# Kernel optimization log

Measured on AMD Instinct MI355X. Metric: run time of the kernel, lower is better.

The kernel has to match this reference:

```python
import jax, jax.numpy as jnp
import numpy as np

N = 50000
E = 800000
IN_C = 256
HID = 256
HEADS = 8
HEAD_C = HID // HEADS
OUT_C = 64
NEG_SLOPE = 0.2  # PyG GATConv default leaky_relu slope


def _glorot(key, shape):
    fan_in = shape[0]
    return jax.random.normal(key, shape, dtype=jnp.float32) / jnp.sqrt(jnp.float32(fan_in))


def setup_inputs() -> dict:
    key = jax.random.key(0)
    ks = jax.random.split(key, 10)
    x = jax.random.normal(ks[0], (N, IN_C), dtype=jnp.float32)
    edge_index = jax.random.randint(ks[1], (2, E), 0, N, dtype=jnp.int32)
    return {
        "x": x,
        "edge_index": edge_index,
        "w1": _glorot(ks[2], (IN_C, HID)),
        "b1": jnp.zeros((HID,), jnp.float32),
        "w_att": _glorot(ks[3], (HID, HEADS * HEAD_C)),
        "att_src": jax.random.normal(ks[4], (HEADS, HEAD_C), dtype=jnp.float32) * 0.1,
        "att_dst": jax.random.normal(ks[5], (HEADS, HEAD_C), dtype=jnp.float32) * 0.1,
        "b_att": jnp.zeros((HEADS * HEAD_C,), jnp.float32),
        "w_mu": _glorot(ks[6], (HID, OUT_C)),
        "b_mu": jnp.zeros((OUT_C,), jnp.float32),
        "w_ls": _glorot(ks[7], (HID, OUT_C)),
        "b_ls": jnp.zeros((OUT_C,), jnp.float32),
    }


def _with_self_loops(edge_index, n):
    loop = jnp.arange(n, dtype=edge_index.dtype)
    src = jnp.concatenate([edge_index[0], loop])
    dst = jnp.concatenate([edge_index[1], loop])
    return src, dst


def gcn_conv(x, w, b, src, dst, n):
    # PyG GCNConv: x' = D^{-1/2} (A+I) D^{-1/2} X W + b
    h = x @ w  # [N, F]
    deg = jax.ops.segment_sum(jnp.ones_like(dst, dtype=h.dtype), dst, num_segments=n)
    dinv = jax.lax.rsqrt(jnp.maximum(deg, 1.0))  # deg >= 1 due to self loops
    norm = dinv[src] * dinv[dst]  # [E']
    msg = h[src] * norm[:, None]
    return jax.ops.segment_sum(msg, dst, num_segments=n) + b


def gat_conv(x, w, att_src, att_dst, b, src, dst, n):
    # PyG GATConv (concat heads, self loops, leaky_relu 0.2, edge softmax by dst)
    h = (x @ w).reshape(n, HEADS, HEAD_C)  # [N, H, C]
    a_src = jnp.einsum('nhc,hc->nh', h, att_src)  # [N, H]
    a_dst = jnp.einsum('nhc,hc->nh', h, att_dst)
    e = jax.nn.leaky_relu(a_src[src] + a_dst[dst], NEG_SLOPE)  # [E', H]
    m = jax.ops.segment_max(e, dst, num_segments=n)  # [N, H]
    e = jnp.exp(e - m[dst])
    s = jax.ops.segment_sum(e, dst, num_segments=n)  # [N, H]
    alpha = e / s[dst]  # [E', H]
    out = jax.ops.segment_sum(h[src] * alpha[:, :, None], dst, num_segments=n)
    return out.reshape(n, HEADS * HEAD_C) + b


def reference(x, edge_index, w1, b1, w_att, att_src, att_dst, b_att, w_mu, b_mu, w_ls, b_ls):
    n = x.shape[0]
    src, dst = _with_self_loops(edge_index, n)
    h = jax.nn.gelu(gcn_conv(x, w1, b1, src, dst, n))
    # dropout is identity at inference
    h = jax.nn.relu(gat_conv(h, w_att, att_src, att_dst, b_att, src, dst, n))
    mu = gcn_conv(h, w_mu, b_mu, src, dst, n)
    logstd = gcn_conv(h, w_ls, b_ls, src, dst, n)
    return mu, logstd
```

## Files before the change

### kernel.cpp

```cpp
#include <hip/hip_runtime.h>

#define NN 50000
#define EE 800000
#define ET (EE + NN)
#define HID 256
#define NH 8
#define HC 32
#define OC 64
#define PC 128

typedef unsigned int u32;
typedef unsigned short u16s;
typedef __bf16 bf16;
typedef _Float16 f16;
typedef __attribute__((ext_vector_type(8))) __bf16 bf16x8;
typedef __attribute__((ext_vector_type(8))) _Float16 f16x8;
typedef __attribute__((ext_vector_type(4))) _Float16 f16x4;
typedef __attribute__((ext_vector_type(4))) float f32x4;

static __device__ __forceinline__ float geluf(float x){
  float t = tanhf(0.7978845608028654f*(x + 0.044715f*x*x*x));
  return 0.5f*x*(1.0f+t);
}
static __device__ __forceinline__ float leakyf(float x){
  return x > 0.0f ? x : 0.2f*x;
}

__global__ void k_init(u32* cnt, u32* counter){
  int i = blockIdx.x*blockDim.x + threadIdx.x;
  if (i < NN) cnt[i] = 1u;
  if (i == 0) counter[0] = 0u;
}
__global__ void k_count(const int* __restrict__ dst, u32* __restrict__ cnt){
  int e = blockIdx.x*blockDim.x + threadIdx.x;
  if (e < EE) atomicAdd(&cnt[dst[e]], 1u);
}
__global__ void k_alloc(const u32* __restrict__ cnt, u32* counter,
                        u32* __restrict__ start, u32* __restrict__ pos,
                        float* __restrict__ dinv){
  int n = blockIdx.x*blockDim.x + threadIdx.x;
  const int lane = threadIdx.x & 63;
  u32 c = (n < NN) ? cnt[n] : 0u;
  u32 pre = c;
  #pragma unroll
  for (int off=1; off<64; off<<=1){
    u32 v = __shfl_up(pre, off);
    if (lane >= off) pre += v;
  }
  u32 tot = __shfl(pre, 63);
  u32 base = 0;
  if (lane == 63) base = atomicAdd(counter, tot);
  base = __shfl(base, 63);
  if (n < NN){
    u32 s = base + pre - c;
    start[n] = s; pos[n] = s;
    dinv[n] = rsqrtf((float)c);
  }
}
__global__ void k_fill(const int* __restrict__ src, const int* __restrict__ dst,
                       u32* __restrict__ pos, u16s* __restrict__ col,
                       const float* __restrict__ dinv, float* __restrict__ nrmE){
  int e = blockIdx.x*blockDim.x + threadIdx.x;
  if (e < ET){
    int s, d;
    if (e < EE){ s = src[e]; d = dst[e]; } else { s = d = e - EE; }
    u32 idx = atomicAdd(&pos[d], 1u);
    col[idx] = (u16s)s;
    nrmE[idx] = dinv[s] * dinv[d];
  }
}

template<int NC>
__global__ void k_wsplit_bf(const float* __restrict__ W, bf16* __restrict__ Whi, bf16* __restrict__ Wlo){
  int e = blockIdx.x*blockDim.x + threadIdx.x;
  if (e >= NC*HID) return;
  int c = e / HID, k = e % HID;
  float w = W[(size_t)k*NC + c];
  bf16 hi = (bf16)w;
  bf16 lo = (bf16)(w - (float)hi);
  Whi[(size_t)c*HID + k] = hi;
  Wlo[(size_t)c*HID + k] = lo;
}
template<int NC>
__global__ void k_wsplit_f16(const float* __restrict__ W, f16* __restrict__ Whi, f16* __restrict__ Wlo, int coff){
  int e = blockIdx.x*blockDim.x + threadIdx.x;
  if (e >= NC*HID) return;
  int c = e / HID, k = e % HID;
  float w = W[(size_t)k*NC + c];
  f16 hi = (f16)w;
  f16 lo = (f16)(w - (float)hi);
  Whi[(size_t)(c+coff)*HID + k] = hi;
  Wlo[(size_t)(c+coff)*HID + k] = lo;
}

template<int NC, int NF, int MR>
__global__ __launch_bounds__(256) void k_gemm_f32A(const float* __restrict__ A,
    const bf16* __restrict__ Whi, const bf16* __restrict__ Wlo, f16* __restrict__ Cout){
  const int tid = threadIdx.x;
  const int w = tid >> 6, lane = tid & 63;
  const int r = lane & 15, g = lane >> 4;
  const int row0 = blockIdx.x * (MR*16);
  const int wcol = w * (NF*16);
  f32x4 acc[MR][NF];
  #pragma unroll
  for (int m=0;m<MR;++m)
    #pragma unroll
    for (int j=0;j<NF;++j){ f32x4 z = {0.f,0.f,0.f,0.f}; acc[m][j] = z; }
  #pragma unroll
  for (int kk=0; kk<8; ++kk){
    const int k0 = kk*32 + g*8;
    bf16x8 ahi[MR], alo[MR];
    #pragma unroll
    for (int m=0;m<MR;++m){
      const int row = row0 + m*16 + r;
      float af[8] = {0.f,0.f,0.f,0.f,0.f,0.f,0.f,0.f};
      if (row < NN){
        const float* ap = A + (size_t)row*HID + k0;
        const float4 u0 = *(const float4*)ap;
        const float4 u1 = *(const float4*)(ap+4);
        af[0]=u0.x; af[1]=u0.y; af[2]=u0.z; af[3]=u0.w;
        af[4]=u1.x; af[5]=u1.y; af[6]=u1.z; af[7]=u1.w;
      }
      #pragma unroll
      for (int i=0;i<8;++i){
        bf16 h = (bf16)af[i];
        ahi[m][i] = h;
        alo[m][i] = (bf16)(af[i] - (float)h);
      }
    }
    #pragma unroll
    for (int j=0;j<NF;++j){
      const int c = wcol + j*16 + r;
      const size_t off = (size_t)c*HID + k0;
      const bf16x8 wh = *(const bf16x8*)(Whi + off);
      const bf16x8 wl = *(const bf16x8*)(Wlo + off);
      #pragma unroll
      for (int m=0;m<MR;++m){
        acc[m][j] = __builtin_amdgcn_mfma_f32_16x16x32_bf16(ahi[m], wh, acc[m][j], 0, 0, 0);
        acc[m][j] = __builtin_amdgcn_mfma_f32_16x16x32_bf16(ahi[m], wl, acc[m][j], 0, 0, 0);
        acc[m][j] = __builtin_amdgcn_mfma_f32_16x16x32_bf16(alo[m], wh, acc[m][j], 0, 0, 0);
      }
    }
  }
  #pragma unroll
  for (int j=0;j<NF;++j){
    const int c = wcol + j*16 + r;
    #pragma unroll
    for (int m=0;m<MR;++m){
      #pragma unroll
      for (int q=0;q<4;++q){
        const int row = row0 + m*16 + g*4 + q;
        if (row < NN) Cout[(size_t)row*NC + c] = (f16)acc[m][j][q];
      }
    }
  }
}

template<int NC, int NF, int MR>
__global__ __launch_bounds__(256) void k_gemm_f16A(const f16* __restrict__ A,
    const f16* __restrict__ Whi, const f16* __restrict__ Wlo, f16* __restrict__ Cout){
  const int tid = threadIdx.x;
  const int w = tid >> 6, lane = tid & 63;
  const int r = lane & 15, g = lane >> 4;
  const int row0 = blockIdx.x * (MR*16);
  const int wcol = w * (NF*16);
  f32x4 acc[MR][NF];
  #pragma unroll
  for (int m=0;m<MR;++m)
    #pragma unroll
    for (int j=0;j<NF;++j){ f32x4 z = {0.f,0.f,0.f,0.f}; acc[m][j] = z; }
  #pragma unroll
  for (int kk=0; kk<8; ++kk){
    const int k0 = kk*32 + g*8;
    f16x8 a[MR];
    #pragma unroll
    for (int m=0;m<MR;++m){
      const int row = row0 + m*16 + r;
      f16x8 z = {0,0,0,0,0,0,0,0};
      a[m] = (row < NN) ? *(const f16x8*)(A + (size_t)row*HID + k0) : z;
    }
    #pragma unroll
    for (int j=0;j<NF;++j){
      const int c = wcol + j*16 + r;
      const size_t off = (size_t)c*HID + k0;
      const f16x8 wh = *(const f16x8*)(Whi + off);
      const f16x8 wl = *(const f16x8*)(Wlo + off);
      #pragma unroll
      for (int m=0;m<MR;++m){
        acc[m][j] = __builtin_amdgcn_mfma_f32_16x16x32_f16(a[m], wh, acc[m][j], 0, 0, 0);
        acc[m][j] = __builtin_amdgcn_mfma_f32_16x16x32_f16(a[m], wl, acc[m][j], 0, 0, 0);
      }
    }
  }
  #pragma unroll
  for (int j=0;j<NF;++j){
    const int c = wcol + j*16 + r;
    #pragma unroll
    for (int m=0;m<MR;++m){
      #pragma unroll
      for (int q=0;q<4;++q){
        const int row = row0 + m*16 + g*4 + q;
        if (row < NN) Cout[(size_t)row*NC + c] = (f16)acc[m][j][q];
      }
    }
  }
}

__global__ __launch_bounds__(256) void k_gemm_att(const f16* __restrict__ A,
    const f16* __restrict__ Whi, const f16* __restrict__ Wlo,
    const float* __restrict__ atts, const float* __restrict__ attd,
    f16* __restrict__ Cout, float* __restrict__ a_src, float* __restrict__ a_dst){
  const int tid = threadIdx.x;
  const int w = tid >> 6, lane = tid & 63;
  const int r = lane & 15, g = lane >> 4;
  const int row0 = blockIdx.x * 64;
  const int wcol = w * 64;
  f32x4 acc[4][4];
  #pragma unroll
  for (int m=0;m<4;++m)
    #pragma unroll
    for (int j=0;j<4;++j){ f32x4 z = {0.f,0.f,0.f,0.f}; acc[m][j] = z; }
  #pragma unroll
  for (int kk=0; kk<8; ++kk){
    const int k0 = kk*32 + g*8;
    f16x8 a[4];
    #pragma unroll
    for (int m=0;m<4;++m){
      const int row = row0 + m*16 + r;
      f16x8 z = {0,0,0,0,0,0,0,0};
      a[m] = (row < NN) ? *(const f16x8*)(A + (size_t)row*HID + k0) : z;
    }
    #pragma unroll
    for (int j=0;j<4;++j){
      const int c = wcol + j*16 + r;
      const size_t off = (size_t)c*HID + k0;
      const f16x8 wh = *(const f16x8*)(Whi + off);
      const f16x8 wl = *(const f16x8*)(Wlo + off);
      #pragma unroll
      for (int m=0;m<4;++m){
        acc[m][j] = __builtin_amdgcn_mfma_f32_16x16x32_f16(a[m], wh, acc[m][j], 0, 0, 0);
        acc[m][j] = __builtin_amdgcn_mfma_f32_16x16x32_f16(a[m], wl, acc[m][j], 0, 0, 0);
      }
    }
  }
  float atv[4], adv[4];
  #pragma unroll
  for (int j=0;j<4;++j){ atv[j] = atts[wcol+j*16+r]; adv[j] = attd[wcol+j*16+r]; }
  #pragma unroll
  for (int m=0;m<4;++m){
    float ps[2][4] = {{0,0,0,0},{0,0,0,0}};
    float pd[2][4] = {{0,0,0,0},{0,0,0,0}};
    #pragma unroll
    for (int j=0;j<4;++j){
      const int c = wcol + j*16 + r;
      const int hl = j >> 1;
      #pragma unroll
      for (int q=0;q<4;++q){
        const int row = row0 + m*16 + g*4 + q;
        const float v = acc[m][j][q];
        if (row < NN) Cout[(size_t)row*HID + c] = (f16)v;
        ps[hl][q] = fmaf(v, atv[j], ps[hl][q]);
        pd[hl][q] = fmaf(v, adv[j], pd[hl][q]);
      }
    }
    #pragma unroll
    for (int hl=0;hl<2;++hl)
      #pragma unroll
      for (int q=0;q<4;++q){
        float s = ps[hl][q], d = pd[hl][q];
        s += __shfl_xor(s,1); s += __shfl_xor(s,2); s += __shfl_xor(s,4); s += __shfl_xor(s,8);
        d += __shfl_xor(d,1); d += __shfl_xor(d,2); d += __shfl_xor(d,4); d += __shfl_xor(d,8);
        if (r == 0){
          const int row = row0 + m*16 + g*4 + q;
          if (row < NN){
            a_src[(size_t)row*NH + 2*w + hl] = s;
            a_dst[(size_t)row*NH + 2*w + hl] = d;
          }
        }
      }
  }
}

__global__ __launch_bounds__(256) void k_aggH(const f16* __restrict__ feat,
    const u16s* __restrict__ col, const u32* __restrict__ start, const u32* __restrict__ cnt,
    const float* __restrict__ nrmE, const float* __restrict__ bias, f16* __restrict__ out){
  const int n = (int)((blockIdx.x*blockDim.x + threadIdx.x) >> 6);
  if (n >= NN) return;
  const int lane = threadIdx.x & 63;
  const u32 b = start[n], e = b + cnt[n];
  const int fo = lane*4;
  float a0=0.f,a1=0.f,a2=0.f,a3=0.f;
  u32 s0 = col[b];
  float w0 = nrmE[b];
  f16x4 v0 = *(const f16x4*)(feat + (size_t)s0*HID + fo);
  for (u32 k=b+1; k<e; ++k){
    const u32 s1 = col[k];
    const float w1 = nrmE[k];
    const f16x4 v1 = *(const f16x4*)(feat + (size_t)s1*HID + fo);
    a0 = fmaf(w0, (float)v0.x, a0);
    a1 = fmaf(w0, (float)v0.y, a1);
    a2 = fmaf(w0, (float)v0.z, a2);
    a3 = fmaf(w0, (float)v0.w, a3);
    v0 = v1; w0 = w1;
  }
  a0 = fmaf(w0, (float)v0.x, a0);
  a1 = fmaf(w0, (float)v0.y, a1);
  a2 = fmaf(w0, (float)v0.z, a2);
  a3 = fmaf(w0, (float)v0.w, a3);
  const float4 bv = *(const float4*)(bias + fo);
  f16x4 o;
  o.x = (f16)geluf(a0 + bv.x);
  o.y = (f16)geluf(a1 + bv.y);
  o.z = (f16)geluf(a2 + bv.z);
  o.w = (f16)geluf(a3 + bv.w);
  *(f16x4*)(out + (size_t)n*HID + fo) = o;
}

__global__ __launch_bounds__(256) void k_gat_fused(const f16* __restrict__ gfeat,
    const u16s* __restrict__ col, const u32* __restrict__ start, const u32* __restrict__ cnt,
    const float* __restrict__ a_src, const float* __restrict__ a_dst,
    const float* __restrict__ b_att, f16* __restrict__ h2){
  const int n = (int)((blockIdx.x*blockDim.x + threadIdx.x) >> 6);
  if (n >= NN) return;
  const int lane = threadIdx.x & 63;
  const int head = lane >> 3;
  const int fo = lane*4;
  const u32 b = start[n], e = b + cnt[n];
  const float ad = a_dst[(size_t)n*NH + head];
  float a0=0.f,a1=0.f,a2=0.f,a3=0.f,sp=0.f;
  u32 s0 = col[b];
  float as0 = a_src[(size_t)s0*NH + head];
  f16x4 v0 = *(const f16x4*)(gfeat + (size_t)s0*HID + fo);
  for (u32 k=b+1; k<e; ++k){
    const u32 s1 = col[k];
    const float as1 = a_src[(size_t)s1*NH + head];
    const f16x4 v1 = *(const f16x4*)(gfeat + (size_t)s1*HID + fo);
    const float p = expf(leakyf(as0 + ad));
    sp += p;
    a0 = fmaf(p, (float)v0.x, a0);
    a1 = fmaf(p, (float)v0.y, a1);
    a2 = fmaf(p, (float)v0.z, a2);
    a3 = fmaf(p, (float)v0.w, a3);
    v0 = v1; as0 = as1;
  }
  const float p = expf(leakyf(as0 + ad));
  sp += p;
  a0 = fmaf(p, (float)v0.x, a0);
  a1 = fmaf(p, (float)v0.y, a1);
  a2 = fmaf(p, (float)v0.z, a2);
  a3 = fmaf(p, (float)v0.w, a3);
  const float inv_s = 1.f / sp;
  const float4 bv = *(const float4*)(b_att + fo);
  f16x4 o;
  o.x = (f16)fmaxf(fmaf(a0, inv_s, bv.x), 0.f);
  o.y = (f16)fmaxf(fmaf(a1, inv_s, bv.y), 0.f);
  o.z = (f16)fmaxf(fmaf(a2, inv_s, bv.z), 0.f);
  o.w = (f16)fmaxf(fmaf(a3, inv_s, bv.w), 0.f);
  *(f16x4*)(h2 + (size_t)n*HID + fo) = o;
}

__global__ __launch_bounds__(256) void k_agg_out(const f16* __restrict__ p,
    const u16s* __restrict__ col, const u32* __restrict__ start, const u32* __restrict__ cnt,
    const float* __restrict__ nrmE, const float* __restrict__ b_mu, const float* __restrict__ b_ls,
    float* __restrict__ out){
  const int n = (int)((blockIdx.x*blockDim.x + threadIdx.x) >> 6);
  if (n >= NN) return;
  const int lane = threadIdx.x & 63;
  const int q4 = lane >> 4, l4 = lane & 15;
  const int fo = l4*8;
  const u32 b = start[n], c = cnt[n];
  float acc[8] = {0.f,0.f,0.f,0.f,0.f,0.f,0.f,0.f};
  u32 i0 = (u32)q4;
  bool v0 = i0 < c;
  u32 idx0 = b + (v0 ? i0 : 0u);
  u32 s0 = col[idx0];
  float nrm0 = v0 ? nrmE[idx0] : 0.f;
  f16x8 f0 = *(const f16x8*)(p + (size_t)s0*PC + fo);
  for (u32 k=4; k<c; k+=4){
    const u32 i1 = k + (u32)q4;
    const bool v1 = i1 < c;
    const u32 idx1 = b + (v1 ? i1 : 0u);
    const u32 s1 = col[idx1];
    const float nrm1 = v1 ? nrmE[idx1] : 0.f;
    const f16x8 f1 = *(const f16x8*)(p + (size_t)s1*PC + fo);
    #pragma unroll
    for (int j=0;j<8;++j) acc[j] = fmaf(nrm0, (float)f0[j], acc[j]);
    f0 = f1; nrm0 = nrm1;
  }
  #pragma unroll
  for (int j=0;j<8;++j) acc[j] = fmaf(nrm0, (float)f0[j], acc[j]);
  #pragma unroll
  for (int j=0;j<8;++j){
    acc[j] += __shfl_xor(acc[j], 16);
    acc[j] += __shfl_xor(acc[j], 32);
  }
  if (q4 == 0){
    if (l4 < 8){
      const int cc = fo;
      float4 o0 = make_float4(acc[0]+b_mu[cc], acc[1]+b_mu[cc+1], acc[2]+b_mu[cc+2], acc[3]+b_mu[cc+3]);
      float4 o1 = make_float4(acc[4]+b_mu[cc+4], acc[5]+b_mu[cc+5], acc[6]+b_mu[cc+6], acc[7]+b_mu[cc+7]);
      *(float4*)(out + (size_t)n*OC + cc) = o0;
      *(float4*)(out + (size_t)n*OC + cc + 4) = o1;
    } else {
      const int cc = fo - OC;
      float* o = out + (size_t)NN*OC + (size_t)n*OC + cc;
      float4 o0 = make_float4(acc[0]+b_ls[cc], acc[1]+b_ls[cc+1], acc[2]+b_ls[cc+2], acc[3]+b_ls[cc+3]);
      float4 o1 = make_float4(acc[4]+b_ls[cc+4], acc[5]+b_ls[cc+5], acc[6]+b_ls[cc+6], acc[7]+b_ls[cc+7]);
      *(float4*)o = o0;
      *(float4*)(o + 4) = o1;
    }
  }
}

extern "C" void kernel_launch(void* const* d_in, const int* in_sizes, int n_in,
                              void* d_out, int out_size, void* d_ws, size_t ws_size,
                              hipStream_t stream){
  const float* x    = (const float*)d_in[0];
  const int*   ei   = (const int*)d_in[1];
  const float* w1   = (const float*)d_in[2];
  const float* b1   = (const float*)d_in[3];
  const float* watt = (const float*)d_in[4];
  const float* atts = (const float*)d_in[5];
  const float* attd = (const float*)d_in[6];
  const float* batt = (const float*)d_in[7];
  const float* wmu  = (const float*)d_in[8];
  const float* bmu  = (const float*)d_in[9];
  const float* wls  = (const float*)d_in[10];
  const float* bls  = (const float*)d_in[11];
  const int* esrc = ei;
  const int* edst = ei + EE;

  char* p = (char*)d_ws;
  f16* bufA = (f16*)p;  p += (size_t)NN*HID*2;
  f16* bufB = (f16*)p;  p += (size_t)NN*HID*2;
  f16* bufC = (f16*)p;  p += (size_t)NN*HID*2;
  float* nrmE = (float*)p; p += (size_t)ET*4;
  bf16* w1hi = (bf16*)p; p += (size_t)HID*HID*2;
  bf16* w1lo = (bf16*)p; p += (size_t)HID*HID*2;
  f16* wahi  = (f16*)p;  p += (size_t)HID*HID*2;
  f16* walo  = (f16*)p;  p += (size_t)HID*HID*2;
  f16* wchi  = (f16*)p;  p += (size_t)PC*HID*2;
  f16* wclo  = (f16*)p;  p += (size_t)PC*HID*2;
  float* dinv = (float*)p; p += (size_t)NN*4;
  float* asr  = (float*)p; p += (size_t)NN*NH*4;
  float* ads  = (float*)p; p += (size_t)NN*NH*4;
  u32*   cnt  = (u32*)p;   p += (size_t)NN*4;
  u32*   start= (u32*)p;   p += (size_t)NN*4;
  u32*   pos  = (u32*)p;   p += (size_t)NN*4;
  u32*   counter = (u32*)p; p += 256;
  u16s*  colU = (u16s*)p;  p += (size_t)ET*2;

  const int TB = 256;
  k_init <<<(NN+TB-1)/TB, TB, 0, stream>>>(cnt, counter);
  k_count<<<(EE+TB-1)/TB, TB, 0, stream>>>(edst, cnt);
  k_alloc<<<(NN+TB-1)/TB, TB, 0, stream>>>(cnt, counter, start, pos, dinv);
  k_fill <<<(ET+TB-1)/TB, TB, 0, stream>>>(esrc, edst, pos, colU, dinv, nrmE);
  k_wsplit_bf<HID><<<(HID*HID+TB-1)/TB, TB, 0, stream>>>(w1, w1hi, w1lo);
  k_wsplit_f16<HID><<<(HID*HID+TB-1)/TB, TB, 0, stream>>>(watt, wahi, walo, 0);
  k_wsplit_f16<OC> <<<(OC*HID+TB-1)/TB, TB, 0, stream>>>(wmu, wchi, wclo, 0);
  k_wsplit_f16<OC> <<<(OC*HID+TB-1)/TB, TB, 0, stream>>>(wls, wchi, wclo, OC);

  const int NWB = NN/4;
  const int G64 = (NN + 63)/64;
  k_gemm_f32A<HID,4,4><<<G64, TB, 0, stream>>>(x, w1hi, w1lo, bufA);
  k_aggH<<<NWB, TB, 0, stream>>>(bufA, colU, start, cnt, nrmE, b1, bufB);
  k_gemm_att<<<G64, TB, 0, stream>>>(bufB, wahi, walo, atts, attd, bufC, asr, ads);
  k_gat_fused<<<NWB, TB, 0, stream>>>(bufC, colU, start, cnt, asr, ads, batt, bufA);
  k_gemm_f16A<PC,2,4><<<G64, TB, 0, stream>>>(bufA, wchi, wclo, bufB);
  k_agg_out<<<NWB, TB, 0, stream>>>(bufB, colU, start, cnt, nrmE, bmu, bls, (float*)d_out);
}
```

Before: 451.5 us.

## Convert x to fp16, merge weight splits, and unroll gather loops by two

```diff
diff --git a/kernel.cpp b/kernel.cpp
--- a/kernel.cpp
+++ b/kernel.cpp
@@ -11,9 +11,7 @@
 
 typedef unsigned int u32;
 typedef unsigned short u16s;
-typedef __bf16 bf16;
 typedef _Float16 f16;
-typedef __attribute__((ext_vector_type(8))) __bf16 bf16x8;
 typedef __attribute__((ext_vector_type(8))) _Float16 f16x8;
 typedef __attribute__((ext_vector_type(4))) _Float16 f16x4;
 typedef __attribute__((ext_vector_type(4))) float f32x4;
@@ -70,90 +68,36 @@
   }
 }
 
-template<int NC>
-__global__ void k_wsplit_bf(const float* __restrict__ W, bf16* __restrict__ Whi, bf16* __restrict__ Wlo){
+__global__ void k_x16(const float* __restrict__ x, f16* __restrict__ o){
+  int i = blockIdx.x*blockDim.x + threadIdx.x;
+  if (i >= NN*HID/8) return;
+  const float4 u0 = *(const float4*)(x + (size_t)i*8);
+  const float4 u1 = *(const float4*)(x + (size_t)i*8 + 4);
+  f16x8 v;
+  v[0]=(f16)u0.x; v[1]=(f16)u0.y; v[2]=(f16)u0.z; v[3]=(f16)u0.w;
+  v[4]=(f16)u1.x; v[5]=(f16)u1.y; v[6]=(f16)u1.z; v[7]=(f16)u1.w;
+  *(f16x8*)(o + (size_t)i*8) = v;
+}
+
+#define W1N (HID*HID)
+__global__ void k_wsplit_all(const float* __restrict__ w1, const float* __restrict__ watt,
+    const float* __restrict__ wmu, const float* __restrict__ wls,
+    f16* __restrict__ w1h, f16* __restrict__ w1l,
+    f16* __restrict__ wah, f16* __restrict__ wal,
+    f16* __restrict__ wch, f16* __restrict__ wcl){
   int e = blockIdx.x*blockDim.x + threadIdx.x;
-  if (e >= NC*HID) return;
-  int c = e / HID, k = e % HID;
-  float w = W[(size_t)k*NC + c];
-  bf16 hi = (bf16)w;
-  bf16 lo = (bf16)(w - (float)hi);
-  Whi[(size_t)c*HID + k] = hi;
-  Wlo[(size_t)c*HID + k] = lo;
-}
-template<int NC>
-__global__ void k_wsplit_f16(const float* __restrict__ W, f16* __restrict__ Whi, f16* __restrict__ Wlo, int coff){
-  int e = blockIdx.x*blockDim.x + threadIdx.x;
-  if (e >= NC*HID) return;
-  int c = e / HID, k = e % HID;
+  const float* W; f16 *H, *L; int NC, coff = 0, idx;
+  if (e < W1N){ W=w1; H=w1h; L=w1l; NC=HID; idx=e; }
+  else if (e < 2*W1N){ W=watt; H=wah; L=wal; NC=HID; idx=e-W1N; }
+  else if (e < 2*W1N + OC*HID){ W=wmu; H=wch; L=wcl; NC=OC; idx=e-2*W1N; }
+  else if (e < 2*W1N + 2*OC*HID){ W=wls; H=wch; L=wcl; NC=OC; coff=OC; idx=e-2*W1N-OC*HID; }
+  else return;
+  int c = idx / HID, k = idx % HID;
   float w = W[(size_t)k*NC + c];
   f16 hi = (f16)w;
   f16 lo = (f16)(w - (float)hi);
-  Whi[(size_t)(c+coff)*HID + k] = hi;
-  Wlo[(size_t)(c+coff)*HID + k] = lo;
-}
-
-template<int NC, int NF, int MR>
-__global__ __launch_bounds__(256) void k_gemm_f32A(const float* __restrict__ A,
-    const bf16* __restrict__ Whi, const bf16* __restrict__ Wlo, f16* __restrict__ Cout){
-  const int tid = threadIdx.x;
-  const int w = tid >> 6, lane = tid & 63;
-  const int r = lane & 15, g = lane >> 4;
-  const int row0 = blockIdx.x * (MR*16);
-  const int wcol = w * (NF*16);
-  f32x4 acc[MR][NF];
-  #pragma unroll
-  for (int m=0;m<MR;++m)
-    #pragma unroll
-    for (int j=0;j<NF;++j){ f32x4 z = {0.f,0.f,0.f,0.f}; acc[m][j] = z; }
-  #pragma unroll
-  for (int kk=0; kk<8; ++kk){
-    const int k0 = kk*32 + g*8;
-    bf16x8 ahi[MR], alo[MR];
-    #pragma unroll
-    for (int m=0;m<MR;++m){
-      const int row = row0 + m*16 + r;
-      float af[8] = {0.f,0.f,0.f,0.f,0.f,0.f,0.f,0.f};
-      if (row < NN){
-        const float* ap = A + (size_t)row*HID + k0;
-        const float4 u0 = *(const float4*)ap;
-        const float4 u1 = *(const float4*)(ap+4);
-        af[0]=u0.x; af[1]=u0.y; af[2]=u0.z; af[3]=u0.w;
-        af[4]=u1.x; af[5]=u1.y; af[6]=u1.z; af[7]=u1.w;
-      }
-      #pragma unroll
-      for (int i=0;i<8;++i){
-        bf16 h = (bf16)af[i];
-        ahi[m][i] = h;
-        alo[m][i] = (bf16)(af[i] - (float)h);
-      }
-    }
-    #pragma unroll
-    for (int j=0;j<NF;++j){
-      const int c = wcol + j*16 + r;
-      const size_t off = (size_t)c*HID + k0;
-      const bf16x8 wh = *(const bf16x8*)(Whi + off);
-      const bf16x8 wl = *(const bf16x8*)(Wlo + off);
-      #pragma unroll
-      for (int m=0;m<MR;++m){
-        acc[m][j] = __builtin_amdgcn_mfma_f32_16x16x32_bf16(ahi[m], wh, acc[m][j], 0, 0, 0);
-        acc[m][j] = __builtin_amdgcn_mfma_f32_16x16x32_bf16(ahi[m], wl, acc[m][j], 0, 0, 0);
-        acc[m][j] = __builtin_amdgcn_mfma_f32_16x16x32_bf16(alo[m], wh, acc[m][j], 0, 0, 0);
-      }
-    }
-  }
-  #pragma unroll
-  for (int j=0;j<NF;++j){
-    const int c = wcol + j*16 + r;
-    #pragma unroll
-    for (int m=0;m<MR;++m){
-      #pragma unroll
-      for (int q=0;q<4;++q){
-        const int row = row0 + m*16 + g*4 + q;
-        if (row < NN) Cout[(size_t)row*NC + c] = (f16)acc[m][j][q];
-      }
-    }
-  }
+  H[(size_t)(c+coff)*HID + k] = hi;
+  L[(size_t)(c+coff)*HID + k] = lo;
 }
 
 template<int NC, int NF, int MR>
@@ -290,23 +234,33 @@
   const u32 b = start[n], e = b + cnt[n];
   const int fo = lane*4;
   float a0=0.f,a1=0.f,a2=0.f,a3=0.f;
+  const u32 k1i = b+1;
+  const bool v1 = k1i < e;
   u32 s0 = col[b];
+  u32 s1 = col[v1 ? k1i : b];
   float w0 = nrmE[b];
-  f16x4 v0 = *(const f16x4*)(feat + (size_t)s0*HID + fo);
-  for (u32 k=b+1; k<e; ++k){
-    const u32 s1 = col[k];
-    const float w1 = nrmE[k];
-    const f16x4 v1 = *(const f16x4*)(feat + (size_t)s1*HID + fo);
-    a0 = fmaf(w0, (float)v0.x, a0);
-    a1 = fmaf(w0, (float)v0.y, a1);
-    a2 = fmaf(w0, (float)v0.z, a2);
-    a3 = fmaf(w0, (float)v0.w, a3);
-    v0 = v1; w0 = w1;
-  }
-  a0 = fmaf(w0, (float)v0.x, a0);
-  a1 = fmaf(w0, (float)v0.y, a1);
-  a2 = fmaf(w0, (float)v0.z, a2);
-  a3 = fmaf(w0, (float)v0.w, a3);
+  float w1 = v1 ? nrmE[k1i] : 0.f;
+  f16x4 r0 = *(const f16x4*)(feat + (size_t)s0*HID + fo);
+  f16x4 r1 = *(const f16x4*)(feat + (size_t)s1*HID + fo);
+  for (u32 k=b+2; k<e; k+=2){
+    const u32 kn = k+1;
+    const bool vv = kn < e;
+    const u32 t0 = col[k];
+    const u32 t1 = col[vv ? kn : k];
+    const float u0 = nrmE[k];
+    const float u1 = vv ? nrmE[kn] : 0.f;
+    const f16x4 q0 = *(const f16x4*)(feat + (size_t)t0*HID + fo);
+    const f16x4 q1 = *(const f16x4*)(feat + (size_t)t1*HID + fo);
+    a0 = fmaf(w0, (float)r0.x, a0); a1 = fmaf(w0, (float)r0.y, a1);
+    a2 = fmaf(w0, (float)r0.z, a2); a3 = fmaf(w0, (float)r0.w, a3);
+    a0 = fmaf(w1, (float)r1.x, a0); a1 = fmaf(w1, (float)r1.y, a1);
+    a2 = fmaf(w1, (float)r1.z, a2); a3 = fmaf(w1, (float)r1.w, a3);
+    r0 = q0; w0 = u0; r1 = q1; w1 = u1;
+  }
+  a0 = fmaf(w0, (float)r0.x, a0); a1 = fmaf(w0, (float)r0.y, a1);
+  a2 = fmaf(w0, (float)r0.z, a2); a3 = fmaf(w0, (float)r0.w, a3);
+  a0 = fmaf(w1, (float)r1.x, a0); a1 = fmaf(w1, (float)r1.y, a1);
+  a2 = fmaf(w1, (float)r1.z, a2); a3 = fmaf(w1, (float)r1.w, a3);
   const float4 bv = *(const float4*)(bias + fo);
   f16x4 o;
   o.x = (f16)geluf(a0 + bv.x);
@@ -328,27 +282,41 @@
   const u32 b = start[n], e = b + cnt[n];
   const float ad = a_dst[(size_t)n*NH + head];
   float a0=0.f,a1=0.f,a2=0.f,a3=0.f,sp=0.f;
+  const u32 k1i = b+1;
+  const bool v1 = k1i < e;
   u32 s0 = col[b];
+  u32 s1 = col[v1 ? k1i : b];
   float as0 = a_src[(size_t)s0*NH + head];
-  f16x4 v0 = *(const f16x4*)(gfeat + (size_t)s0*HID + fo);
-  for (u32 k=b+1; k<e; ++k){
-    const u32 s1 = col[k];
-    const float as1 = a_src[(size_t)s1*NH + head];
-    const f16x4 v1 = *(const f16x4*)(gfeat + (size_t)s1*HID + fo);
-    const float p = expf(leakyf(as0 + ad));
-    sp += p;
-    a0 = fmaf(p, (float)v0.x, a0);
-    a1 = fmaf(p, (float)v0.y, a1);
-    a2 = fmaf(p, (float)v0.z, a2);
-    a3 = fmaf(p, (float)v0.w, a3);
-    v0 = v1; as0 = as1;
-  }
-  const float p = expf(leakyf(as0 + ad));
-  sp += p;
-  a0 = fmaf(p, (float)v0.x, a0);
-  a1 = fmaf(p, (float)v0.y, a1);
-  a2 = fmaf(p, (float)v0.z, a2);
-  a3 = fmaf(p, (float)v0.w, a3);
+  float as1 = v1 ? a_src[(size_t)s1*NH + head] : -1e30f;
+  f16x4 r0 = *(const f16x4*)(gfeat + (size_t)s0*HID + fo);
+  f16x4 r1 = *(const f16x4*)(gfeat + (size_t)s1*HID + fo);
+  for (u32 k=b+2; k<e; k+=2){
+    const u32 kn = k+1;
+    const bool vv = kn < e;
+    const u32 t0 = col[k];
+    const u32 t1 = col[vv ? kn : k];
+    const float at0 = a_src[(size_t)t0*NH + head];
+    const float at1 = vv ? a_src[(size_t)t1*NH + head] : -1e30f;
+    const f16x4 q0 = *(const f16x4*)(gfeat + (size_t)t0*HID + fo);
+    const f16x4 q1 = *(const f16x4*)(gfeat + (size_t)t1*HID + fo);
+    const float p0 = expf(leakyf(as0 + ad));
+    sp += p0;
+    a0 = fmaf(p0, (float)r0.x, a0); a1 = fmaf(p0, (float)r0.y, a1);
+    a2 = fmaf(p0, (float)r0.z, a2); a3 = fmaf(p0, (float)r0.w, a3);
+    const float p1 = expf(leakyf(as1 + ad));
+    sp += p1;
+    a0 = fmaf(p1, (float)r1.x, a0); a1 = fmaf(p1, (float)r1.y, a1);
+    a2 = fmaf(p1, (float)r1.z, a2); a3 = fmaf(p1, (float)r1.w, a3);
+    r0 = q0; as0 = at0; r1 = q1; as1 = at1;
+  }
+  const float p0 = expf(leakyf(as0 + ad));
+  sp += p0;
+  a0 = fmaf(p0, (float)r0.x, a0); a1 = fmaf(p0, (float)r0.y, a1);
+  a2 = fmaf(p0, (float)r0.z, a2); a3 = fmaf(p0, (float)r0.w, a3);
+  const float p1 = expf(leakyf(as1 + ad));
+  sp += p1;
+  a0 = fmaf(p1, (float)r1.x, a0); a1 = fmaf(p1, (float)r1.y, a1);
+  a2 = fmaf(p1, (float)r1.z, a2); a3 = fmaf(p1, (float)r1.w, a3);
   const float inv_s = 1.f / sp;
   const float4 bv = *(const float4*)(b_att + fo);
   f16x4 o;
@@ -435,8 +403,8 @@
   f16* bufB = (f16*)p;  p += (size_t)NN*HID*2;
   f16* bufC = (f16*)p;  p += (size_t)NN*HID*2;
   float* nrmE = (float*)p; p += (size_t)ET*4;
-  bf16* w1hi = (bf16*)p; p += (size_t)HID*HID*2;
-  bf16* w1lo = (bf16*)p; p += (size_t)HID*HID*2;
+  f16* w1h   = (f16*)p;  p += (size_t)HID*HID*2;
+  f16* w1l   = (f16*)p;  p += (size_t)HID*HID*2;
   f16* wahi  = (f16*)p;  p += (size_t)HID*HID*2;
   f16* walo  = (f16*)p;  p += (size_t)HID*HID*2;
   f16* wchi  = (f16*)p;  p += (size_t)PC*HID*2;
@@ -455,14 +423,13 @@
   k_count<<<(EE+TB-1)/TB, TB, 0, stream>>>(edst, cnt);
   k_alloc<<<(NN+TB-1)/TB, TB, 0, stream>>>(cnt, counter, start, pos, dinv);
   k_fill <<<(ET+TB-1)/TB, TB, 0, stream>>>(esrc, edst, pos, colU, dinv, nrmE);
-  k_wsplit_bf<HID><<<(HID*HID+TB-1)/TB, TB, 0, stream>>>(w1, w1hi, w1lo);
-  k_wsplit_f16<HID><<<(HID*HID+TB-1)/TB, TB, 0, stream>>>(watt, wahi, walo, 0);
-  k_wsplit_f16<OC> <<<(OC*HID+TB-1)/TB, TB, 0, stream>>>(wmu, wchi, wclo, 0);
-  k_wsplit_f16<OC> <<<(OC*HID+TB-1)/TB, TB, 0, stream>>>(wls, wchi, wclo, OC);
+  k_wsplit_all<<<(2*W1N + 2*OC*HID + TB-1)/TB, TB, 0, stream>>>(
+      w1, watt, wmu, wls, w1h, w1l, wahi, walo, wchi, wclo);
+  k_x16<<<(NN*HID/8 + TB-1)/TB, TB, 0, stream>>>(x, bufC);
 
   const int NWB = NN/4;
   const int G64 = (NN + 63)/64;
-  k_gemm_f32A<HID,4,4><<<G64, TB, 0, stream>>>(x, w1hi, w1lo, bufA);
+  k_gemm_f16A<HID,4,4><<<G64, TB, 0, stream>>>(bufC, w1h, w1l, bufA);
   k_aggH<<<NWB, TB, 0, stream>>>(bufA, colU, start, cnt, nrmE, b1, bufB);
   k_gemm_att<<<G64, TB, 0, stream>>>(bufB, wahi, walo, atts, attd, bufC, asr, ads);
   k_gat_fused<<<NWB, TB, 0, stream>>>(bufC, colU, start, cnt, asr, ads, batt, bufA);
```

Measured after the change: 440.7 us. 1.02x faster.

## Switch first GEMM to fp16 two-term split, merge weight splits, memset init

Applied to the files above, without the earlier changes.

```diff
diff --git a/kernel.cpp b/kernel.cpp
--- a/kernel.cpp
+++ b/kernel.cpp
@@ -11,9 +11,7 @@
 
 typedef unsigned int u32;
 typedef unsigned short u16s;
-typedef __bf16 bf16;
 typedef _Float16 f16;
-typedef __attribute__((ext_vector_type(8))) __bf16 bf16x8;
 typedef __attribute__((ext_vector_type(8))) _Float16 f16x8;
 typedef __attribute__((ext_vector_type(4))) _Float16 f16x4;
 typedef __attribute__((ext_vector_type(4))) float f32x4;
@@ -26,21 +24,16 @@
   return x > 0.0f ? x : 0.2f*x;
 }
 
-__global__ void k_init(u32* cnt, u32* counter){
-  int i = blockIdx.x*blockDim.x + threadIdx.x;
-  if (i < NN) cnt[i] = 1u;
-  if (i == 0) counter[0] = 0u;
-}
 __global__ void k_count(const int* __restrict__ dst, u32* __restrict__ cnt){
   int e = blockIdx.x*blockDim.x + threadIdx.x;
   if (e < EE) atomicAdd(&cnt[dst[e]], 1u);
 }
-__global__ void k_alloc(const u32* __restrict__ cnt, u32* counter,
+__global__ void k_alloc(u32* __restrict__ cnt, u32* counter,
                         u32* __restrict__ start, u32* __restrict__ pos,
                         float* __restrict__ dinv){
   int n = blockIdx.x*blockDim.x + threadIdx.x;
   const int lane = threadIdx.x & 63;
-  u32 c = (n < NN) ? cnt[n] : 0u;
+  u32 c = (n < NN) ? (cnt[n] + 1u) : 0u;
   u32 pre = c;
   #pragma unroll
   for (int off=1; off<64; off<<=1){
@@ -55,6 +48,7 @@
     u32 s = base + pre - c;
     start[n] = s; pos[n] = s;
     dinv[n] = rsqrtf((float)c);
+    cnt[n] = c;
   }
 }
 __global__ void k_fill(const int* __restrict__ src, const int* __restrict__ dst,
@@ -70,32 +64,30 @@
   }
 }
 
-template<int NC>
-__global__ void k_wsplit_bf(const float* __restrict__ W, bf16* __restrict__ Whi, bf16* __restrict__ Wlo){
+#define W1N (HID*HID)
+__global__ void k_wsplit_all(const float* __restrict__ w1, const float* __restrict__ watt,
+    const float* __restrict__ wmu, const float* __restrict__ wls,
+    f16* __restrict__ w1h, f16* __restrict__ w1l,
+    f16* __restrict__ wah, f16* __restrict__ wal,
+    f16* __restrict__ wch, f16* __restrict__ wcl){
   int e = blockIdx.x*blockDim.x + threadIdx.x;
-  if (e >= NC*HID) return;
-  int c = e / HID, k = e % HID;
-  float w = W[(size_t)k*NC + c];
-  bf16 hi = (bf16)w;
-  bf16 lo = (bf16)(w - (float)hi);
-  Whi[(size_t)c*HID + k] = hi;
-  Wlo[(size_t)c*HID + k] = lo;
-}
-template<int NC>
-__global__ void k_wsplit_f16(const float* __restrict__ W, f16* __restrict__ Whi, f16* __restrict__ Wlo, int coff){
-  int e = blockIdx.x*blockDim.x + threadIdx.x;
-  if (e >= NC*HID) return;
-  int c = e / HID, k = e % HID;
+  const float* W; f16 *H, *L; int NC, coff = 0, idx;
+  if (e < W1N){ W=w1; H=w1h; L=w1l; NC=HID; idx=e; }
+  else if (e < 2*W1N){ W=watt; H=wah; L=wal; NC=HID; idx=e-W1N; }
+  else if (e < 2*W1N + OC*HID){ W=wmu; H=wch; L=wcl; NC=OC; idx=e-2*W1N; }
+  else if (e < 2*W1N + 2*OC*HID){ W=wls; H=wch; L=wcl; NC=OC; coff=OC; idx=e-2*W1N-OC*HID; }
+  else return;
+  int c = idx / HID, k = idx % HID;
   float w = W[(size_t)k*NC + c];
   f16 hi = (f16)w;
   f16 lo = (f16)(w - (float)hi);
-  Whi[(size_t)(c+coff)*HID + k] = hi;
-  Wlo[(size_t)(c+coff)*HID + k] = lo;
+  H[(size_t)(c+coff)*HID + k] = hi;
+  L[(size_t)(c+coff)*HID + k] = lo;
 }
 
 template<int NC, int NF, int MR>
-__global__ __launch_bounds__(256) void k_gemm_f32A(const float* __restrict__ A,
-    const bf16* __restrict__ Whi, const bf16* __restrict__ Wlo, f16* __restrict__ Cout){
+__global__ __launch_bounds__(256) void k_gemm_fx(const float* __restrict__ A,
+    const f16* __restrict__ Whi, const f16* __restrict__ Wlo, f16* __restrict__ Cout){
   const int tid = threadIdx.x;
   const int w = tid >> 6, lane = tid & 63;
   const int r = lane & 15, g = lane >> 4;
@@ -109,36 +101,30 @@
   #pragma unroll
   for (int kk=0; kk<8; ++kk){
     const int k0 = kk*32 + g*8;
-    bf16x8 ahi[MR], alo[MR];
+    f16x8 a[MR];
     #pragma unroll
     for (int m=0;m<MR;++m){
       const int row = row0 + m*16 + r;
-      float af[8] = {0.f,0.f,0.f,0.f,0.f,0.f,0.f,0.f};
+      f16x8 v = {0,0,0,0,0,0,0,0};
       if (row < NN){
         const float* ap = A + (size_t)row*HID + k0;
         const float4 u0 = *(const float4*)ap;
         const float4 u1 = *(const float4*)(ap+4);
-        af[0]=u0.x; af[1]=u0.y; af[2]=u0.z; af[3]=u0.w;
-        af[4]=u1.x; af[5]=u1.y; af[6]=u1.z; af[7]=u1.w;
-      }
-      #pragma unroll
-      for (int i=0;i<8;++i){
-        bf16 h = (bf16)af[i];
-        ahi[m][i] = h;
-        alo[m][i] = (bf16)(af[i] - (float)h);
-      }
+        v[0]=(f16)u0.x; v[1]=(f16)u0.y; v[2]=(f16)u0.z; v[3]=(f16)u0.w;
+        v[4]=(f16)u1.x; v[5]=(f16)u1.y; v[6]=(f16)u1.z; v[7]=(f16)u1.w;
+      }
+      a[m] = v;
     }
     #pragma unroll
     for (int j=0;j<NF;++j){
       const int c = wcol + j*16 + r;
       const size_t off = (size_t)c*HID + k0;
-      const bf16x8 wh = *(const bf16x8*)(Whi + off);
-      const bf16x8 wl = *(const bf16x8*)(Wlo + off);
+      const f16x8 wh = *(const f16x8*)(Whi + off);
+      const f16x8 wl = *(const f16x8*)(Wlo + off);
       #pragma unroll
       for (int m=0;m<MR;++m){
-        acc[m][j] = __builtin_amdgcn_mfma_f32_16x16x32_bf16(ahi[m], wh, acc[m][j], 0, 0, 0);
-        acc[m][j] = __builtin_amdgcn_mfma_f32_16x16x32_bf16(ahi[m], wl, acc[m][j], 0, 0, 0);
-        acc[m][j] = __builtin_amdgcn_mfma_f32_16x16x32_bf16(alo[m], wh, acc[m][j], 0, 0, 0);
+        acc[m][j] = __builtin_amdgcn_mfma_f32_16x16x32_f16(a[m], wh, acc[m][j], 0, 0, 0);
+        acc[m][j] = __builtin_amdgcn_mfma_f32_16x16x32_f16(a[m], wl, acc[m][j], 0, 0, 0);
       }
     }
   }
@@ -435,8 +421,8 @@
   f16* bufB = (f16*)p;  p += (size_t)NN*HID*2;
   f16* bufC = (f16*)p;  p += (size_t)NN*HID*2;
   float* nrmE = (float*)p; p += (size_t)ET*4;
-  bf16* w1hi = (bf16*)p; p += (size_t)HID*HID*2;
-  bf16* w1lo = (bf16*)p; p += (size_t)HID*HID*2;
+  f16* w1h   = (f16*)p;  p += (size_t)HID*HID*2;
+  f16* w1l   = (f16*)p;  p += (size_t)HID*HID*2;
   f16* wahi  = (f16*)p;  p += (size_t)HID*HID*2;
   f16* walo  = (f16*)p;  p += (size_t)HID*HID*2;
   f16* wchi  = (f16*)p;  p += (size_t)PC*HID*2;
@@ -451,18 +437,18 @@
   u16s*  colU = (u16s*)p;  p += (size_t)ET*2;
 
   const int TB = 256;
-  k_init <<<(NN+TB-1)/TB, TB, 0, stream>>>(cnt, counter);
+  hipMemsetAsync(cnt, 0, (size_t)NN*4, stream);
+  hipMemsetAsync(counter, 0, 4, stream);
   k_count<<<(EE+TB-1)/TB, TB, 0, stream>>>(edst, cnt);
   k_alloc<<<(NN+TB-1)/TB, TB, 0, stream>>>(cnt, counter, start, pos, dinv);
   k_fill <<<(ET+TB-1)/TB, TB, 0, stream>>>(esrc, edst, pos, colU, dinv, nrmE);
-  k_wsplit_bf<HID><<<(HID*HID+TB-1)/TB, TB, 0, stream>>>(w1, w1hi, w1lo);
-  k_wsplit_f16<HID><<<(HID*HID+TB-1)/TB, TB, 0, stream>>>(watt, wahi, walo, 0);
-  k_wsplit_f16<OC> <<<(OC*HID+TB-1)/TB, TB, 0, stream>>>(wmu, wchi, wclo, 0);
-  k_wsplit_f16<OC> <<<(OC*HID+TB-1)/TB, TB, 0, stream>>>(wls, wchi, wclo, OC);
+  k_wsplit_all<<<(2*W1N + 2*OC*HID + TB-1)/TB, TB, 0, stream>>>(
+      w1, watt, wmu, wls, w1h, w1l, wahi, walo, wchi, wclo);
 
   const int NWB = NN/4;
   const int G64 = (NN + 63)/64;
-  k_gemm_f32A<HID,4,4><<<G64, TB, 0, stream>>>(x, w1hi, w1lo, bufA);
+  const int G128 = (NN + 127)/128;
+  k_gemm_fx<HID,4,8><<<G128, TB, 0, stream>>>(x, w1h, w1l, bufA);
   k_aggH<<<NWB, TB, 0, stream>>>(bufA, colU, start, cnt, nrmE, b1, bufB);
   k_gemm_att<<<G64, TB, 0, stream>>>(bufB, wahi, walo, atts, attd, bufC, asr, ads);
   k_gat_fused<<<NWB, TB, 0, stream>>>(bufC, colU, start, cnt, asr, ads, batt, bufA);
```

After: 463.1 us. 1.03x slower.
